# Optimization experiments

Hardware: AMD Instinct MI355X
Metric: run time of the kernel (lower is better)

Reference implementation:

```python
import jax, jax.numpy as jnp
import numpy as np

H = 64    # encoder/decoder hidden size
L = 10    # num_lags
D = 128   # input_dim (features)
OUT = 5   # out_dim
B = 8192


def lstm_cell(x, h, c, Wih, Whh, bih, bhh):
    # torch nn.LSTM gate order: i, f, g, o
    g = x @ Wih.T + bih + h @ Whh.T + bhh
    i, f, gg, o = jnp.split(g, 4, axis=-1)
    c = jax.nn.sigmoid(f) * c + jax.nn.sigmoid(i) * jnp.tanh(gg)
    h = jax.nn.sigmoid(o) * jnp.tanh(c)
    return h, c


def setup_inputs() -> dict:
    key = jax.random.key(0)
    ks = jax.random.split(key, 24)
    rn = lambda k, s, sc=0.05: jax.random.normal(k, s, jnp.float32) * sc
    return {
        "x": rn(ks[0], (B, L, D), 1.0),
        "y_hist": rn(ks[1], (B, L, OUT), 1.0),
        "h0_enc": rn(ks[2], (B, H), 0.1),
        "c0_enc": rn(ks[3], (B, H), 0.1),
        "h0_dec": rn(ks[4], (B, H), 0.1),
        "c0_dec": rn(ks[5], (B, H), 0.1),
        # encoder attention: Linear(2H+L -> 1)
        "enc_attn_w": rn(ks[6], (1, 2 * H + L)),
        "enc_attn_b": rn(ks[7], (1,)),
        # encoder LSTM
        "enc_Wih": rn(ks[8], (4 * H, D)),
        "enc_Whh": rn(ks[9], (4 * H, H)),
        "enc_bih": rn(ks[10], (4 * H,)),
        "enc_bhh": rn(ks[11], (4 * H,)),
        # decoder attention MLP: Linear(3H -> H), tanh, Linear(H -> 1)
        "dec_attn_w1": rn(ks[12], (H, 3 * H)),
        "dec_attn_b1": rn(ks[13], (H,)),
        "dec_attn_w2": rn(ks[14], (1, H)),
        "dec_attn_b2": rn(ks[15], (1,)),
        # decoder LSTM (input = out_dim)
        "dec_Wih": rn(ks[16], (4 * H, OUT)),
        "dec_Whh": rn(ks[17], (4 * H, H)),
        "dec_bih": rn(ks[18], (4 * H,)),
        "dec_bhh": rn(ks[19], (4 * H,)),
        # fc: Linear(H+OUT -> OUT)  (weight .normal_() in torch -> std 1)
        "fc_w": rn(ks[20], (OUT, H + OUT), 1.0),
        "fc_b": rn(ks[21], (OUT,)),
        # fc_out: Linear(2H -> OUT)
        "fcout_w": rn(ks[22], (OUT, 2 * H)),
        "fcout_b": rn(ks[23], (OUT,)),
    }


def reference(x, y_hist, h0_enc, c0_enc, h0_dec, c0_dec,
              enc_attn_w, enc_attn_b, enc_Wih, enc_Whh, enc_bih, enc_bhh,
              dec_attn_w1, dec_attn_b1, dec_attn_w2, dec_attn_b2,
              dec_Wih, dec_Whh, dec_bih, dec_bhh, fc_w, fc_b, fcout_w, fcout_b):
    # ---- encoder (input attention over features) ----
    # Linear([h; c; x_feat_series]) = wh.h + wc.c + wx.x_series + b
    wh, wc, wx = enc_attn_w[0, :H], enc_attn_w[0, H:2 * H], enc_attn_w[0, 2 * H:]
    score_x = jnp.einsum('bdl,l->bd', jnp.transpose(x, (0, 2, 1)), wx)  # [B, D]

    def enc_step(carry, x_t):
        h, c = carry
        scores = (h @ wh + c @ wc)[:, None] + score_x + enc_attn_b[0]   # [B, D]
        at = jax.nn.softmax(scores, axis=1)
        wi = at * x_t                                                   # [B, D]
        h, c = lstm_cell(wi, h, c, enc_Wih, enc_Whh, enc_bih, enc_bhh)
        return (h, c), h

    _, enc_seq = jax.lax.scan(enc_step, (h0_enc, c0_enc), jnp.transpose(x, (1, 0, 2)))
    x_enc = jnp.transpose(enc_seq, (1, 0, 2))                           # [B, L, H]

    # ---- decoder (temporal attention over encoded lags) ----
    W1h, W1c, W1x = dec_attn_w1[:, :H], dec_attn_w1[:, H:2 * H], dec_attn_w1[:, 2 * H:]
    pre = jnp.einsum('ble,he->blh', x_enc, W1x)                         # [B, L, H]
    w2 = dec_attn_w2[0]

    def dec_step(carry, y_t):
        h, c, _ = carry
        z = jnp.tanh(pre + (h @ W1h.T + c @ W1c.T + dec_attn_b1)[:, None, :])
        scores = z @ w2 + dec_attn_b2[0]                                # [B, L]
        at = jax.nn.softmax(scores, axis=1)
        ctx = jnp.einsum('bl,ble->be', at, x_enc)                       # [B, H]
        y_tilde = jnp.concatenate([ctx, y_t], axis=1) @ fc_w.T + fc_b   # [B, OUT]
        h, c = lstm_cell(y_tilde, h, c, dec_Wih, dec_Whh, dec_bih, dec_bhh)
        return (h, c, ctx), None

    (h, c, ctx), _ = jax.lax.scan(
        dec_step, (h0_dec, c0_dec, jnp.zeros_like(h0_dec)),
        jnp.transpose(y_hist, (1, 0, 2)))
    out = jnp.concatenate([h, ctx], axis=1) @ fcout_w.T + fcout_b       # [B, OUT]
    return out
```

## Files before the change

### kernel.cpp

```cpp
#include <hip/hip_runtime.h>

#define B_  8192
#define L_  10
#define D_  128
#define H_  64
#define OUT_ 5

typedef _Float16 h2 __attribute__((ext_vector_type(2)));
typedef _Float16 f16x8 __attribute__((ext_vector_type(8)));
typedef float f32x4 __attribute__((ext_vector_type(4)));
typedef unsigned int uint;

#define WS_ENCPK   0
#define WS_ENCB    24576
#define WS_DECY2   24832
#define WS_DECPK   26112
#define WS_DECB    34304
#define WS_W1HCP   34560
#define WS_W1XP    38656

__device__ __forceinline__ float sigmf(float x){ return 1.f/(1.f+__expf(-x)); }
__device__ __forceinline__ float tanhf_(float x){ return 1.f - 2.f/(1.f+__expf(2.f*x)); }
__device__ __forceinline__ uint pack_rtz(float a, float b){
  return __builtin_bit_cast(uint, __builtin_amdgcn_cvt_pkrtz(a, b));
}
__device__ __forceinline__ uint pack_rtn(float a, float b){
  h2 v; v.x = (_Float16)a; v.y = (_Float16)b;
  return __builtin_bit_cast(uint, v);
}
__device__ __forceinline__ float2 unpk(uint u){
  h2 v = __builtin_bit_cast(h2, u);
  return make_float2((float)v.x, (float)v.y);
}

union U4 { uint u[4]; uint4 q; f16x8 v; };

__global__ void prep_kernel(const float* __restrict__ encWih, const float* __restrict__ encWhh,
                            const float* __restrict__ encbih, const float* __restrict__ encbhh,
                            const float* __restrict__ decWih, const float* __restrict__ decWhh,
                            const float* __restrict__ decbih, const float* __restrict__ decbhh,
                            const float* __restrict__ w1, float* __restrict__ wsf)
{
  uint* ws = (uint*)wsf;
  int stride = gridDim.x * blockDim.x;
  int tid0 = blockIdx.x * blockDim.x + threadIdx.x;

  for (int idx = tid0; idx < 96*64; idx += stride) {
    int kp = idx >> 6, l = idx & 63;
    uint4 o; uint* op = (uint*)&o;
    #pragma unroll
    for (int q=0;q<4;++q){
      int j = q*64 + l;
      int k0 = 2*kp, k1 = 2*kp+1;
      float a = (k0 < 128) ? encWih[j*128 + k0] : encWhh[j*64 + (k0-128)];
      float b = (k1 < 128) ? encWih[j*128 + k1] : encWhh[j*64 + (k1-128)];
      op[q] = pack_rtn(a,b);
    }
    ((uint4*)(ws + WS_ENCPK))[idx] = o;
  }
  for (int idx = tid0; idx < 256; idx += stride) {
    int l = idx >> 2, q = idx & 3, j = q*64+l;
    wsf[WS_ENCB+idx] = encbih[j] + encbhh[j];
  }
  for (int idx = tid0; idx < 4*64; idx += stride) {
    int i = idx >> 6, l = idx & 63;
    uint4 o; uint* op = (uint*)&o;
    #pragma unroll
    for (int q=0;q<4;++q){
      int j = q*64 + l;
      int k0 = 2*i, k1 = 2*i+1;
      float a = (k0 < 5) ? decWih[j*5 + k0] : 0.f;
      float b = (k1 < 5) ? decWih[j*5 + k1] : 0.f;
      op[q] = pack_rtn(a,b);
    }
    ((uint4*)(ws + WS_DECY2))[idx] = o;
  }
  for (int idx = tid0; idx < 32*64; idx += stride) {
    int ep = idx >> 6, l = idx & 63;
    uint4 o; uint* op = (uint*)&o;
    #pragma unroll
    for (int q=0;q<4;++q){
      int j = q*64 + l;
      op[q] = pack_rtn(decWhh[j*64 + 2*ep], decWhh[j*64 + 2*ep+1]);
    }
    ((uint4*)(ws + WS_DECPK))[idx] = o;
  }
  for (int idx = tid0; idx < 256; idx += stride) {
    int l = idx >> 2, q = idx & 3, j = q*64+l;
    wsf[WS_DECB+idx] = decbih[j] + decbhh[j];
  }
  for (int idx = tid0; idx < 32*64; idx += stride) {
    int ep = idx >> 6, l = idx & 63;
    uint2 o;
    o.x = pack_rtn(w1[l*192 + 2*ep],      w1[l*192 + 2*ep+1]);
    o.y = pack_rtn(w1[l*192 + 64 + 2*ep], w1[l*192 + 64 + 2*ep+1]);
    ((uint2*)(ws + WS_W1HCP))[idx] = o;
  }
  for (int idx = tid0; idx < 32*64; idx += stride) {
    int ep = idx >> 6, l = idx & 63;
    ws[WS_W1XP + idx] = pack_rtn(w1[l*192 + 128 + 2*ep], w1[l*192 + 128 + 2*ep+1]);
  }
}

#define SM_HXE   0
#define SM_XES   4608
#define SM_TMPF  0
#define SM_TMPG  12800
#define SM_HXD   27648
#define SM_CXD   32256
#define SM_SRED  36864
#define SM_FXE   39424
#define SM_GXE   42624
#define SM_YBS   45824
#define SM_TOTAL 49024

__global__ __launch_bounds__(256)
__attribute__((amdgpu_waves_per_eu(2, 2)))
void darnn_fused(
    const float* __restrict__ x, const float* __restrict__ enc_attn_w,
    const float* __restrict__ y_hist,
    const float* __restrict__ h0e, const float* __restrict__ c0e,
    const float* __restrict__ h0d, const float* __restrict__ c0d,
    const float* __restrict__ dec_attn_b1, const float* __restrict__ dec_attn_w2,
    const float* __restrict__ fc_w, const float* __restrict__ fc_b,
    const float* __restrict__ fcout_w, const float* __restrict__ fcout_b,
    const float* __restrict__ ws,
    float* __restrict__ out)
{
  const int tid = threadIdx.x;
  const int l   = tid & 63;
  const int w   = tid >> 6;
  const int col = l & 15;
  const int g   = l >> 4;
  const int b0  = blockIdx.x * 16;
  const int lw  = 16*w + col;
  const int u0  = 16*w + 4*g;

  const uint* wsu = (const uint*)ws;

  __shared__ __align__(16) char smem_[SM_TOTAL];
  _Float16 (*wiS)[16][136] = reinterpret_cast<_Float16(*)[16][136]>(smem_);
  uint     (*hxE)[16][36] = reinterpret_cast<uint(*)[16][36]>(smem_ + SM_HXE);
  _Float16 (*xeS)[16][72] = reinterpret_cast<_Float16(*)[16][72]>(smem_ + SM_XES);
  float* tmpF = (float*)(smem_ + SM_TMPF);
  float* tmpG = (float*)(smem_ + SM_TMPG);
  uint     (*hxD)[16][36] = reinterpret_cast<uint(*)[16][36]>(smem_ + SM_HXD);
  uint     (*cxD)[16][36] = reinterpret_cast<uint(*)[16][36]>(smem_ + SM_CXD);
  float* sred = (float*)(smem_ + SM_SRED);
  float* fxeS = (float*)(smem_ + SM_FXE);
  float* gxeS = (float*)(smem_ + SM_GXE);
  float* ybS  = (float*)(smem_ + SM_YBS);

  if (tid < 200){
    float4 yreg = *(const float4*)(y_hist + (size_t)b0*50 + tid*4);
    *(float4*)(ybS + tid*4) = yreg;
  }
  float4 hd4 = *(const float4*)(h0d + (size_t)(b0+col)*64 + u0);
  float4 cd4 = *(const float4*)(c0d + (size_t)(b0+col)*64 + u0);
  float4 he4 = *(const float4*)(h0e + (size_t)(b0+col)*64 + u0);
  float4 ce4 = *(const float4*)(c0e + (size_t)(b0+col)*64 + u0);

  f16x8 afr[4][4];
  #pragma unroll
  for (int im=0; im<4; ++im){
    #pragma unroll
    for (int kf=0; kf<4; ++kf){
      U4 cv;
      #pragma unroll
      for (int i=0;i<4;++i){
        int kp = kf*16 + g*4 + i;
        cv.u[i] = wsu[WS_ENCPK + (kp*64 + lw)*4 + im];
      }
      afr[im][kf] = cv.v;
    }
  }
  float bias[4][4];
  #pragma unroll
  for (int im=0; im<4; ++im)
    #pragma unroll
    for (int r=0; r<4; ++r)
      bias[im][r] = ws[WS_ENCB + (u0 + r)*4 + im];

  const int bb = tid >> 4;
  const int kc = tid & 15;
  const float* xb = x + (size_t)(b0+bb)*(L_*D_) + kc*8;

  float wxv[L_];
  #pragma unroll
  for (int t=0;t<L_;++t) wxv[t] = enc_attn_w[2*H_ + t];

  float s[8];
  #pragma unroll
  for (int j=0;j<8;++j) s[j]=0.f;
  #pragma unroll
  for (int t=0;t<L_;++t){
    float wx = wxv[t];
    float4 x0 = *(const float4*)(xb + t*D_);
    float4 x1 = *(const float4*)(xb + t*D_ + 4);
    s[0]+=x0.x*wx; s[1]+=x0.y*wx; s[2]+=x0.z*wx; s[3]+=x0.w*wx;
    s[4]+=x1.x*wx; s[5]+=x1.y*wx; s[6]+=x1.z*wx; s[7]+=x1.w*wx;
  }
  float m = s[0];
  #pragma unroll
  for (int j=1;j<8;++j) m = fmaxf(m, s[j]);
  m = fmaxf(m, __shfl_xor(m,1));
  m = fmaxf(m, __shfl_xor(m,2));
  m = fmaxf(m, __shfl_xor(m,4));
  m = fmaxf(m, __shfl_xor(m,8));
  float atw[8];
  float ss = 0.f;
  #pragma unroll
  for (int j=0;j<8;++j){ atw[j] = __expf(s[j]-m); ss += atw[j]; }
  ss += __shfl_xor(ss,1);
  ss += __shfl_xor(ss,2);
  ss += __shfl_xor(ss,4);
  ss += __shfl_xor(ss,8);
  float ainv = 1.f/ss;
  #pragma unroll
  for (int j=0;j<8;++j) atw[j] *= ainv;

  #pragma unroll
  for (int t=0;t<L_;++t){
    float4 x0 = *(const float4*)(xb + t*D_);
    float4 x1 = *(const float4*)(xb + t*D_ + 4);
    uint4 o;
    o.x = pack_rtz(atw[0]*x0.x, atw[1]*x0.y);
    o.y = pack_rtz(atw[2]*x0.z, atw[3]*x0.w);
    o.z = pack_rtz(atw[4]*x1.x, atw[5]*x1.y);
    o.w = pack_rtz(atw[6]*x1.z, atw[7]*x1.w);
    *(uint4*)&wiS[t][bb][kc*8] = o;
  }
  __syncthreads();

  uint2 gq[L_][4];
  #pragma unroll
  for (int t=0;t<L_;++t){
    U4 bu[4];
    #pragma unroll
    for (int kf=0;kf<4;++kf)
      bu[kf].q = *(const uint4*)&wiS[t][col][kf*32 + g*8];
    #pragma unroll
    for (int im=0;im<4;++im){
      f32x4 acc = { bias[im][0], bias[im][1], bias[im][2], bias[im][3] };
      #pragma unroll
      for (int kf=0;kf<4;++kf)
        acc = __builtin_amdgcn_mfma_f32_16x16x32_f16(afr[im][kf], bu[kf].v, acc, 0, 0, 0);
      gq[t][im] = make_uint2(pack_rtn(acc[0],acc[1]), pack_rtn(acc[2],acc[3]));
    }
  }
  __syncthreads();

  f16x8 aE[4][2];
  #pragma unroll
  for (int q=0;q<4;++q)
    #pragma unroll
    for (int kf=0;kf<2;++kf){
      U4 cv;
      #pragma unroll
      for (int i=0;i<4;++i)
        cv.u[i] = wsu[WS_ENCPK + ((64 + kf*16 + g*4 + i)*64 + lw)*4 + q];
      aE[q][kf] = cv.v;
    }

  float h[4], c[4], xer[L_][4];
  h[0]=he4.x; h[1]=he4.y; h[2]=he4.z; h[3]=he4.w;
  c[0]=ce4.x; c[1]=ce4.y; c[2]=ce4.z; c[3]=ce4.w;
  *(uint2*)&hxE[0][col][u0>>1] = make_uint2(pack_rtz(h[0],h[1]), pack_rtz(h[2],h[3]));
  __syncthreads();

  int p = 0;
  #pragma unroll
  for (int t=0; t<L_; ++t){
    f32x4 acc[4];
    #pragma unroll
    for (int q=0;q<4;++q){
      float2 u0f = unpk(gq[t][q].x), u1f = unpk(gq[t][q].y);
      acc[q][0]=u0f.x; acc[q][1]=u0f.y; acc[q][2]=u1f.x; acc[q][3]=u1f.y;
    }
    f16x8 hB[2];
    { U4 t0; t0.q = *(const uint4*)&hxE[p][col][g*4];      hB[0]=t0.v; }
    { U4 t1; t1.q = *(const uint4*)&hxE[p][col][16 + g*4]; hB[1]=t1.v; }

    #pragma unroll
    for (int q=0;q<4;++q){
      acc[q] = __builtin_amdgcn_mfma_f32_16x16x32_f16(aE[q][0], hB[0], acc[q], 0,0,0);
      acc[q] = __builtin_amdgcn_mfma_f32_16x16x32_f16(aE[q][1], hB[1], acc[q], 0,0,0);
    }
    #pragma unroll
    for (int r=0;r<4;++r){
      float ig=sigmf(acc[0][r]), fg=sigmf(acc[1][r]), gg=tanhf_(acc[2][r]), og=sigmf(acc[3][r]);
      c[r]=fg*c[r]+ig*gg;
      h[r]=og*tanhf_(c[r]);
      xer[t][r]=h[r];
    }
    uint2 hpk = make_uint2(pack_rtz(h[0],h[1]), pack_rtz(h[2],h[3]));
    *(uint2*)&xeS[t][col][u0] = hpk;
    *(uint2*)&hxE[p^1][col][u0>>1] = hpk;
    __syncthreads();
    p ^= 1;
  }

  f16x8 aX[2];
  #pragma unroll
  for (int kf=0;kf<2;++kf){
    U4 cv;
    #pragma unroll
    for (int i=0;i<4;++i) cv.u[i] = wsu[WS_W1XP + (kf*16 + g*4 + i)*64 + lw];
    aX[kf] = cv.v;
  }
  f32x4 preC[L_];
  #pragma unroll
  for (int lt=0;lt<L_;++lt){
    f32x4 a = {0.f,0.f,0.f,0.f};
    U4 bu0, bu1;
    bu0.q = *(const uint4*)&xeS[lt][col][g*8];
    bu1.q = *(const uint4*)&xeS[lt][col][32 + g*8];
    a = __builtin_amdgcn_mfma_f32_16x16x32_f16(aX[0], bu0.v, a, 0,0,0);
    a = __builtin_amdgcn_mfma_f32_16x16x32_f16(aX[1], bu1.v, a, 0,0,0);
    preC[lt] = a;
  }
  __syncthreads();

  {
    float fw1v[OUT_][4], gw1v[OUT_][4];
    #pragma unroll
    for (int o2=0;o2<OUT_;++o2)
      #pragma unroll
      for (int r=0;r<4;++r){
        fw1v[o2][r] = fc_w[o2*69 + u0 + r];
        gw1v[o2][r] = fcout_w[o2*128 + 64 + u0 + r];
      }
    #pragma unroll
    for (int lt=0;lt<L_;++lt){
      #pragma unroll
      for (int o2=0;o2<OUT_;++o2){
        float pf = fw1v[o2][0]*xer[lt][0] + fw1v[o2][1]*xer[lt][1]
                 + fw1v[o2][2]*xer[lt][2] + fw1v[o2][3]*xer[lt][3];
        float pg = gw1v[o2][0]*xer[lt][0] + gw1v[o2][1]*xer[lt][1]
                 + gw1v[o2][2]*xer[lt][2] + gw1v[o2][3]*xer[lt][3];
        pf += __shfl_xor(pf,16); pf += __shfl_xor(pf,32);
        pg += __shfl_xor(pg,16); pg += __shfl_xor(pg,32);
        if (g==0){
          tmpF[((lt*16+col)*OUT_+o2)*4 + w] = pf;
          tmpG[((lt*16+col)*OUT_+o2)*4 + w] = pg;
        }
      }
    }
  }
  __syncthreads();
  for (int idx=tid; idx<800; idx+=256){
    float4 f4 = *(const float4*)(tmpF + idx*4);
    float4 g4 = *(const float4*)(tmpG + idx*4);
    int o2 = idx % 5, rest = idx / 5;
    int b  = rest % 16, lt = rest / 16;
    fxeS[b*50 + lt*5 + o2] = f4.x+f4.y+f4.z+f4.w;
    gxeS[b*50 + lt*5 + o2] = g4.x+g4.y+g4.z+g4.w;
  }

  f16x8 aW1[4];
  #pragma unroll
  for (int kf=0;kf<4;++kf){
    U4 cv;
    #pragma unroll
    for (int i=0;i<4;++i){
      int ep = (kf&1)*16 + g*4 + i;
      cv.u[i] = wsu[WS_W1HCP + (ep*64 + lw)*2 + (kf>>1)];
    }
    aW1[kf] = cv.v;
  }
  f16x8 aGh[4][2];
  #pragma unroll
  for (int q=0;q<4;++q)
    #pragma unroll
    for (int kf=0;kf<2;++kf){
      U4 cv;
      #pragma unroll
      for (int i=0;i<4;++i)
        cv.u[i] = wsu[WS_DECPK + ((kf*16 + g*4 + i)*64 + lw)*4 + q];
      aGh[q][kf] = cv.v;
    }
  f16x8 aG0[4];
  #pragma unroll
  for (int q=0;q<4;++q){
    U4 cv;
    #pragma unroll
    for (int i=0;i<4;++i)
      cv.u[i] = (g==0) ? wsu[WS_DECY2 + (i*64 + lw)*4 + q] : 0u;
    aG0[q] = cv.v;
  }
  float4 bD[4];
  #pragma unroll
  for (int r=0;r<4;++r) bD[r] = *(const float4*)(ws + WS_DECB + (u0+r)*4);
  float4 b1v = *(const float4*)(dec_attn_b1 + u0);
  float4 w2v = *(const float4*)(dec_attn_w2 + u0);
  float fcbv[OUT_], fw2v[OUT_][OUT_];
  #pragma unroll
  for (int o2=0;o2<OUT_;++o2){
    fcbv[o2] = fc_b[o2];
    #pragma unroll
    for (int j=0;j<OUT_;++j) fw2v[o2][j] = fc_w[o2*69 + 64 + j];
  }

  h[0]=hd4.x; h[1]=hd4.y; h[2]=hd4.z; h[3]=hd4.w;
  c[0]=cd4.x; c[1]=cd4.y; c[2]=cd4.z; c[3]=cd4.w;
  *(uint2*)&hxD[0][col][u0>>1] = make_uint2(pack_rtz(h[0],h[1]), pack_rtz(h[2],h[3]));
  *(uint2*)&cxD[0][col][u0>>1] = make_uint2(pack_rtz(c[0],c[1]), pack_rtz(c[2],c[3]));
  __syncthreads();

  float at[L_];
  float inv = 0.f;
  p = 0;
  for (int t=0; t<L_; ++t){
    f16x8 hB[2], cB[2];
    { U4 t0; t0.q = *(const uint4*)&hxD[p][col][g*4];      hB[0]=t0.v; }
    { U4 t1; t1.q = *(const uint4*)&hxD[p][col][16 + g*4]; hB[1]=t1.v; }
    { U4 t2; t2.q = *(const uint4*)&cxD[p][col][g*4];      cB[0]=t2.v; }
    { U4 t3; t3.q = *(const uint4*)&cxD[p][col][16 + g*4]; cB[1]=t3.v; }

    f32x4 vb = { b1v.x, b1v.y, b1v.z, b1v.w };
    vb = __builtin_amdgcn_mfma_f32_16x16x32_f16(aW1[0], hB[0], vb, 0,0,0);
    vb = __builtin_amdgcn_mfma_f32_16x16x32_f16(aW1[1], hB[1], vb, 0,0,0);
    vb = __builtin_amdgcn_mfma_f32_16x16x32_f16(aW1[2], cB[0], vb, 0,0,0);
    vb = __builtin_amdgcn_mfma_f32_16x16x32_f16(aW1[3], cB[1], vb, 0,0,0);

    #pragma unroll
    for (int lt=0;lt<L_;++lt){
      float zp = tanhf_(preC[lt][0] + vb[0]) * w2v.x
               + tanhf_(preC[lt][1] + vb[1]) * w2v.y
               + tanhf_(preC[lt][2] + vb[2]) * w2v.z
               + tanhf_(preC[lt][3] + vb[3]) * w2v.w;
      zp += __shfl_xor(zp,16);
      zp += __shfl_xor(zp,32);
      at[lt] = zp;
    }
    if (g==0){
      #pragma unroll
      for (int lt=0;lt<L_;++lt) sred[(lt*16+col)*4 + w] = at[lt];
    }
    __syncthreads();
    #pragma unroll
    for (int lt=0;lt<L_;++lt){
      float4 s4 = *(const float4*)(sred + (lt*16+col)*4);
      at[lt] = s4.x + s4.y + s4.z + s4.w;
    }
    float mx = at[0];
    #pragma unroll
    for (int lt=1;lt<L_;++lt) mx = fmaxf(mx, at[lt]);
    float ssum = 0.f;
    #pragma unroll
    for (int lt=0;lt<L_;++lt){ at[lt] = __expf(at[lt]-mx); ssum += at[lt]; }
    inv = 1.f/ssum;

    U4 ycv; ycv.u[0]=0u; ycv.u[1]=0u; ycv.u[2]=0u; ycv.u[3]=0u;
    if (g==0){
      const float* fx = fxeS + col*50;
      const float* yb = ybS + col*50 + t*5;
      float yt[OUT_];
      #pragma unroll
      for (int o2=0;o2<OUT_;++o2){
        float sv = 0.f;
        #pragma unroll
        for (int lt=0;lt<L_;++lt) sv += at[lt]*fx[lt*5+o2];
        float v = sv*inv + fcbv[o2];
        #pragma unroll
        for (int j=0;j<OUT_;++j) v += yb[j]*fw2v[o2][j];
        yt[o2] = v;
      }
      ycv.u[0] = pack_rtn(yt[0], yt[1]);
      ycv.u[1] = pack_rtn(yt[2], yt[3]);
      ycv.u[2] = pack_rtn(yt[4], 0.f);
    }
    f32x4 accQ[4];
    #pragma unroll
    for (int q=0;q<4;++q){
      accQ[q][0]=((const float*)&bD[0])[q];
      accQ[q][1]=((const float*)&bD[1])[q];
      accQ[q][2]=((const float*)&bD[2])[q];
      accQ[q][3]=((const float*)&bD[3])[q];
    }
    #pragma unroll
    for (int q=0;q<4;++q){
      accQ[q] = __builtin_amdgcn_mfma_f32_16x16x32_f16(aG0[q], ycv.v, accQ[q], 0,0,0);
      accQ[q] = __builtin_amdgcn_mfma_f32_16x16x32_f16(aGh[q][0], hB[0], accQ[q], 0,0,0);
      accQ[q] = __builtin_amdgcn_mfma_f32_16x16x32_f16(aGh[q][1], hB[1], accQ[q], 0,0,0);
    }
    #pragma unroll
    for (int r=0;r<4;++r){
      float ig=sigmf(accQ[0][r]), fg=sigmf(accQ[1][r]), gg=tanhf_(accQ[2][r]), og=sigmf(accQ[3][r]);
      c[r]=fg*c[r]+ig*gg;
      h[r]=og*tanhf_(c[r]);
    }
    *(uint2*)&hxD[p^1][col][u0>>1] = make_uint2(pack_rtz(h[0],h[1]), pack_rtz(h[2],h[3]));
    *(uint2*)&cxD[p^1][col][u0>>1] = make_uint2(pack_rtz(c[0],c[1]), pack_rtz(c[2],c[3]));
    __syncthreads();
    p ^= 1;
  }

  {
    float fcA[OUT_][4];
    #pragma unroll
    for (int o2=0;o2<OUT_;++o2)
      #pragma unroll
      for (int r=0;r<4;++r) fcA[o2][r] = fcout_w[o2*128 + u0 + r];
    #pragma unroll
    for (int o2=0;o2<OUT_;++o2){
      float pv = fcA[o2][0]*h[0] + fcA[o2][1]*h[1] + fcA[o2][2]*h[2] + fcA[o2][3]*h[3];
      pv += __shfl_xor(pv,16);
      pv += __shfl_xor(pv,32);
      if (g==0) sred[(o2*16+col)*4 + w] = pv;
    }
  }
  __syncthreads();
  if (w==0 && g==0){
    const float* gx = gxeS + col*50;
    #pragma unroll
    for (int o2=0;o2<OUT_;++o2){
      float4 s4 = *(const float4*)(sred + (o2*16+col)*4);
      float sv = 0.f;
      #pragma unroll
      for (int lt=0;lt<L_;++lt) sv += at[lt]*gx[lt*5+o2];
      out[(size_t)(b0+col)*OUT_ + o2] = s4.x+s4.y+s4.z+s4.w + sv*inv + fcout_b[o2];
    }
  }
}

extern "C" void kernel_launch(void* const* d_in, const int* in_sizes, int n_in,
                              void* d_out, int out_size, void* d_ws, size_t ws_size,
                              hipStream_t stream) {
  const float* x          = (const float*)d_in[0];
  const float* y_hist     = (const float*)d_in[1];
  const float* h0_enc     = (const float*)d_in[2];
  const float* c0_enc     = (const float*)d_in[3];
  const float* h0_dec     = (const float*)d_in[4];
  const float* c0_dec     = (const float*)d_in[5];
  const float* enc_attn_w = (const float*)d_in[6];
  const float* enc_Wih    = (const float*)d_in[8];
  const float* enc_Whh    = (const float*)d_in[9];
  const float* enc_bih    = (const float*)d_in[10];
  const float* enc_bhh    = (const float*)d_in[11];
  const float* dec_attn_w1= (const float*)d_in[12];
  const float* dec_attn_b1= (const float*)d_in[13];
  const float* dec_attn_w2= (const float*)d_in[14];
  const float* dec_Wih    = (const float*)d_in[16];
  const float* dec_Whh    = (const float*)d_in[17];
  const float* dec_bih    = (const float*)d_in[18];
  const float* dec_bhh    = (const float*)d_in[19];
  const float* fc_w       = (const float*)d_in[20];
  const float* fc_b       = (const float*)d_in[21];
  const float* fcout_w    = (const float*)d_in[22];
  const float* fcout_b    = (const float*)d_in[23];
  float* ws = (float*)d_ws;
  float* out = (float*)d_out;

  hipLaunchKernelGGL(prep_kernel, dim3(128), dim3(256), 0, stream,
                     enc_Wih, enc_Whh, enc_bih, enc_bhh,
                     dec_Wih, dec_Whh, dec_bih, dec_bhh,
                     dec_attn_w1, ws);
  hipLaunchKernelGGL(darnn_fused, dim3(B_/16), dim3(256), 0, stream,
                     x, enc_attn_w, y_hist,
                     h0_enc, c0_enc, h0_dec, c0_dec,
                     dec_attn_b1, dec_attn_w2,
                     fc_w, fc_b, fcout_w, fcout_b, ws, out);
}
```

Baseline: 218.2 us.

## Split decoder softmax/context across lane groups and hoist hidden-state gate MFMAs

Each of the four 16-lane groups now computes exp scores for up to three lags and reduces partial softmax sums and context-weighted fc terms by cross-lane shuffles. Previously one group did the full ten-lag loop serially. The hidden-state part of the LSTM gate MFMAs is issued right after the attention MFMAs, so it can overlap with the tanh/softmax work. The max subtraction in softmax is dropped, which relies on the scores being bounded. The time loop is fully unrolled and the final attention weights are recomputed after the loop, which adds an extra barrier.

```diff
diff --git a/kernel.cpp b/kernel.cpp
--- a/kernel.cpp
+++ b/kernel.cpp
@@ -114,8 +114,7 @@
 #define SM_YBS   45824
 #define SM_TOTAL 49024
 
-__global__ __launch_bounds__(256)
-__attribute__((amdgpu_waves_per_eu(2, 2)))
+__global__ __launch_bounds__(256, 2)
 void darnn_fused(
     const float* __restrict__ x, const float* __restrict__ enc_attn_w,
     const float* __restrict__ y_hist,
@@ -407,9 +406,14 @@
   *(uint2*)&cxD[0][col][u0>>1] = make_uint2(pack_rtz(c[0],c[1]), pack_rtz(c[2],c[3]));
   __syncthreads();
 
-  float at[L_];
-  float inv = 0.f;
+  const int lt0 = g*3;
+  const int lt1c = (lt0+1 < L_) ? lt0+1 : 0;
+  const int lt2c = (lt0+2 < L_) ? lt0+2 : 0;
+  const bool v1 = (lt0+1 < L_), v2 = (lt0+2 < L_);
+  const float* fx = fxeS + col*50;
+
   p = 0;
+  #pragma unroll
   for (int t=0; t<L_; ++t){
     f16x8 hB[2], cB[2];
     { U4 t0; t0.q = *(const uint4*)&hxD[p][col][g*4];      hB[0]=t0.v; }
@@ -422,6 +426,20 @@
     vb = __builtin_amdgcn_mfma_f32_16x16x32_f16(aW1[1], hB[1], vb, 0,0,0);
     vb = __builtin_amdgcn_mfma_f32_16x16x32_f16(aW1[2], cB[0], vb, 0,0,0);
     vb = __builtin_amdgcn_mfma_f32_16x16x32_f16(aW1[3], cB[1], vb, 0,0,0);
+
+    f32x4 accQ[4];
+    #pragma unroll
+    for (int q=0;q<4;++q){
+      accQ[q][0]=((const float*)&bD[0])[q];
+      accQ[q][1]=((const float*)&bD[1])[q];
+      accQ[q][2]=((const float*)&bD[2])[q];
+      accQ[q][3]=((const float*)&bD[3])[q];
+    }
+    #pragma unroll
+    for (int q=0;q<4;++q){
+      accQ[q] = __builtin_amdgcn_mfma_f32_16x16x32_f16(aGh[q][0], hB[0], accQ[q], 0,0,0);
+      accQ[q] = __builtin_amdgcn_mfma_f32_16x16x32_f16(aGh[q][1], hB[1], accQ[q], 0,0,0);
+    }
 
     #pragma unroll
     for (int lt=0;lt<L_;++lt){
@@ -431,37 +449,35 @@
                + tanhf_(preC[lt][3] + vb[3]) * w2v.w;
       zp += __shfl_xor(zp,16);
       zp += __shfl_xor(zp,32);
-      at[lt] = zp;
-    }
-    if (g==0){
-      #pragma unroll
-      for (int lt=0;lt<L_;++lt) sred[(lt*16+col)*4 + w] = at[lt];
+      if (g==0) sred[(lt*16+col)*4 + w] = zp;
     }
     __syncthreads();
-    #pragma unroll
-    for (int lt=0;lt<L_;++lt){
-      float4 s4 = *(const float4*)(sred + (lt*16+col)*4);
-      at[lt] = s4.x + s4.y + s4.z + s4.w;
-    }
-    float mx = at[0];
-    #pragma unroll
-    for (int lt=1;lt<L_;++lt) mx = fmaxf(mx, at[lt]);
-    float ssum = 0.f;
-    #pragma unroll
-    for (int lt=0;lt<L_;++lt){ at[lt] = __expf(at[lt]-mx); ssum += at[lt]; }
-    inv = 1.f/ssum;
+
+    float e0, e1, e2;
+    { float4 s4 = *(const float4*)(sred + (lt0 *16+col)*4); e0 = __expf(s4.x+s4.y+s4.z+s4.w); }
+    { float4 s4 = *(const float4*)(sred + (lt1c*16+col)*4); e1 = v1 ? __expf(s4.x+s4.y+s4.z+s4.w) : 0.f; }
+    { float4 s4 = *(const float4*)(sred + (lt2c*16+col)*4); e2 = v2 ? __expf(s4.x+s4.y+s4.z+s4.w) : 0.f; }
+    float psum = e0 + e1 + e2;
+    psum += __shfl_xor(psum,16);
+    psum += __shfl_xor(psum,32);
+    float inv = 1.f/psum;
+
+    float svv[OUT_];
+    #pragma unroll
+    for (int o2=0;o2<OUT_;++o2){
+      float sv = e0*fx[lt0*5+o2] + e1*fx[lt1c*5+o2] + e2*fx[lt2c*5+o2];
+      sv += __shfl_xor(sv,16);
+      sv += __shfl_xor(sv,32);
+      svv[o2] = sv;
+    }
 
     U4 ycv; ycv.u[0]=0u; ycv.u[1]=0u; ycv.u[2]=0u; ycv.u[3]=0u;
     if (g==0){
-      const float* fx = fxeS + col*50;
       const float* yb = ybS + col*50 + t*5;
       float yt[OUT_];
       #pragma unroll
       for (int o2=0;o2<OUT_;++o2){
-        float sv = 0.f;
-        #pragma unroll
-        for (int lt=0;lt<L_;++lt) sv += at[lt]*fx[lt*5+o2];
-        float v = sv*inv + fcbv[o2];
+        float v = svv[o2]*inv + fcbv[o2];
         #pragma unroll
         for (int j=0;j<OUT_;++j) v += yb[j]*fw2v[o2][j];
         yt[o2] = v;
@@ -470,20 +486,10 @@
       ycv.u[1] = pack_rtn(yt[2], yt[3]);
       ycv.u[2] = pack_rtn(yt[4], 0.f);
     }
-    f32x4 accQ[4];
-    #pragma unroll
-    for (int q=0;q<4;++q){
-      accQ[q][0]=((const float*)&bD[0])[q];
-      accQ[q][1]=((const float*)&bD[1])[q];
-      accQ[q][2]=((const float*)&bD[2])[q];
-      accQ[q][3]=((const float*)&bD[3])[q];
-    }
-    #pragma unroll
-    for (int q=0;q<4;++q){
+    #pragma unroll
+    for (int q=0;q<4;++q)
       accQ[q] = __builtin_amdgcn_mfma_f32_16x16x32_f16(aG0[q], ycv.v, accQ[q], 0,0,0);
-      accQ[q] = __builtin_amdgcn_mfma_f32_16x16x32_f16(aGh[q][0], hB[0], accQ[q], 0,0,0);
-      accQ[q] = __builtin_amdgcn_mfma_f32_16x16x32_f16(aGh[q][1], hB[1], accQ[q], 0,0,0);
-    }
+
     #pragma unroll
     for (int r=0;r<4;++r){
       float ig=sigmf(accQ[0][r]), fg=sigmf(accQ[1][r]), gg=tanhf_(accQ[2][r]), og=sigmf(accQ[3][r]);
@@ -495,6 +501,19 @@
     __syncthreads();
     p ^= 1;
   }
+
+  float atE[L_], invE;
+  {
+    float ssumE = 0.f;
+    #pragma unroll
+    for (int lt=0; lt<L_; ++lt){
+      float4 s4 = *(const float4*)(sred + (lt*16+col)*4);
+      atE[lt] = __expf(s4.x+s4.y+s4.z+s4.w);
+      ssumE += atE[lt];
+    }
+    invE = 1.f/ssumE;
+  }
+  __syncthreads();
 
   {
     float fcA[OUT_][4];
@@ -518,8 +537,8 @@
       float4 s4 = *(const float4*)(sred + (o2*16+col)*4);
       float sv = 0.f;
       #pragma unroll
-      for (int lt=0;lt<L_;++lt) sv += at[lt]*gx[lt*5+o2];
-      out[(size_t)(b0+col)*OUT_ + o2] = s4.x+s4.y+s4.z+s4.w + sv*inv + fcout_b[o2];
+      for (int lt=0;lt<L_;++lt) sv += atE[lt]*gx[lt*5+o2];
+      out[(size_t)(b0+col)*OUT_ + o2] = s4.x+s4.y+s4.z+s4.w + sv*invE + fcout_b[o2];
     }
   }
 }
```

Measured after the change: 218.1 us. About the same (-0.0%).
